# Optimization experiments

Measured on AMD Instinct MI355X. Metric: run time of the kernel, lower is better.

## Reference

```python
import jax, jax.numpy as jnp
import numpy as np

B, T, O = 64, 2048, 3          # batch, window_len, overlap (O >= ngram_n-1)
D, V = 512, 128                # embed_dim, vocab_size
M, NG, H = 100000, 4, 4        # engram memory_size, ngram_n, engram/sgrm num_heads
HD = D // H                    # head_dim = 128
PAD = 0
EPS_RMS = 1e-6


def _engram_primes():
    # per-head rolling-hash primes, exactly as in MultiHeadEngram.setup
    ps = []
    base = 131
    for h in range(H):
        x = base + h * 1009
        row = []
        for _ in range(NG):
            row.append(x)
            x = x * 31 + 1
        ps.append(row)
    return jnp.asarray(np.array(ps, dtype=np.uint32))  # (H, NG)


def setup_inputs() -> dict:
    key = jax.random.key(0)
    ks = jax.random.split(key, 10)
    tokens_w = jax.random.randint(ks[0], (B, T), 0, V, dtype=jnp.int32)
    prev_ids_overlap = jax.random.randint(ks[1], (B, O), 0, V, dtype=jnp.int32)
    mask_bool = jax.random.randint(ks[2], (B, T), 0, 2) > 0
    embed_table = jax.random.normal(ks[3], (V, D), jnp.float32) * 0.02
    engram_table = jax.random.normal(ks[4], (M, H, HD), jnp.float32) * 0.02
    gate_logit = jnp.full((H, HD), -2.0, jnp.float32)
    temp = jnp.ones((H,), jnp.float32)
    sal_W = jax.random.normal(ks[5], (D, H), jnp.float32) * 0.02
    sal_b = jnp.zeros((H,), jnp.float32)
    gate_W = jax.random.normal(ks[6], (HD, 1), jnp.float32) * 0.02
    gate_b = jnp.zeros((1,), jnp.float32)
    rms_scale = jnp.ones((D,), jnp.float32)
    return {"tokens_w": tokens_w, "prev_ids_overlap": prev_ids_overlap,
            "mask_bool": mask_bool, "embed_table": embed_table,
            "engram_table": engram_table, "gate_logit": gate_logit,
            "temp": temp, "sal_W": sal_W, "sal_b": sal_b,
            "gate_W": gate_W, "gate_b": gate_b, "rms_scale": rms_scale}


def reference(tokens_w, prev_ids_overlap, mask_bool, embed_table, engram_table,
              gate_logit, temp, sal_W, sal_b, gate_W, gate_b, rms_scale):
    # ---- MultiHeadEngram: hashed n-gram multi-head gather + sigmoid gate ----
    cur = jnp.where(tokens_w == PAD, 0, tokens_w)
    prv = jnp.where(prev_ids_overlap == PAD, 0, prev_ids_overlap)
    full_seq = jnp.concatenate([prv, cur], axis=1).astype(jnp.uint32)  # (B, O+T)
    primes = _engram_primes()                                          # (H, NG)
    hash_sums = jnp.zeros((B, T, H), dtype=jnp.uint32)
    for i in range(NG):  # rolling n-gram hash (uint32 wraparound)
        chunk = full_seq[:, O - i: O + T - i]                          # (B, T)
        hash_sums = hash_sums + chunk[:, :, None] * primes[None, None, :, i]
    lookup = (hash_sums % M).astype(jnp.int32)                         # (B, T, H)
    # per-head gather: row lookup[b,t,h] of head h's table slice
    retrieved = engram_table[lookup, jnp.arange(H)[None, None, :], :]  # (B, T, H, HD)
    gate = jax.nn.sigmoid(gate_logit)                                  # (H, HD)
    engram_out = (retrieved * gate[None, None]).reshape(B, T, D)

    # token embedding + engram injection (dropout is identity: deterministic)
    x = embed_table[tokens_w] + engram_out                             # (B, T, D)

    # ---- SalienceWriteHead: masked softmax temporal pooling + gating ----
    x_heads = x.reshape(B, T, H, HD)
    temperature = jax.nn.softplus(temp) + 0.3                          # (H,)
    logits = (x @ sal_W + sal_b) / temperature[None, None, :]          # (B, T, H)
    m = mask_bool[:, :, None]
    safe_logits = jnp.where(m, logits, -1e9)
    max_logits = jax.lax.stop_gradient(jnp.max(safe_logits, axis=1, keepdims=True))
    exps = jnp.where(m, jnp.exp(safe_logits - max_logits), 0.0)
    weights = exps / (jnp.sum(exps, axis=1, keepdims=True) + 1e-6)     # (B, T, H)
    write_vec_heads = jnp.einsum('bth,bthd->bhd', weights, x_heads)    # (B, H, HD)
    gate_logits = write_vec_heads @ gate_W + gate_b                    # (B, H, 1)
    window_valid = jnp.any(mask_bool, axis=1)[:, None, None]
    write_u_heads = jax.nn.sigmoid(gate_logits) * window_valid.astype(jnp.float32)
    write_vec = write_vec_heads.reshape(B, D)
    # RMSNorm
    rms = jnp.sqrt(jnp.mean(jnp.square(write_vec), axis=-1, keepdims=True) + EPS_RMS)
    write_vec = write_vec / rms * rms_scale
    write_u_expanded = jnp.tile(write_u_heads, (1, 1, HD)).reshape(B, D)
    return jnp.concatenate([write_vec, write_u_expanded], axis=-1)     # (B, 2D)
```

## Files before the change

kernel.cpp:

```cpp
#include <hip/hip_runtime.h>
#include <stdint.h>

#define B_ 64
#define T_ 2048
#define O_ 3
#define D_ 512
#define V_ 128
#define M_ 100000
#define H_ 4
#define HD_ 128

__device__ __constant__ unsigned PRIMES_c[H_][4] = {
  {131u,  4062u,  125923u, 3903614u},
  {1140u, 35341u, 1095572u, 33962733u},
  {2149u, 66620u, 2065221u, 64021852u},
  {3158u, 97899u, 3034870u, 94080971u},
};

template<int CTRL, int RMASK>
__device__ __forceinline__ float dpp_term(float x) {
  return __int_as_float(__builtin_amdgcn_update_dpp(
      0, __float_as_int(x), CTRL, RMASK, 0xF, true));
}

__device__ __forceinline__ float wave_sum(float x) {
  x += dpp_term<0xB1, 0xF>(x);
  x += dpp_term<0x4E, 0xF>(x);
  x += dpp_term<0x141, 0xF>(x);
  x += dpp_term<0x140, 0xF>(x);
  x += dpp_term<0x142, 0xA>(x);
  x += dpp_term<0x143, 0xC>(x);
  return __int_as_float(__builtin_amdgcn_readlane(__float_as_int(x), 63));
}

__device__ __forceinline__ bool read_mask(const void* mb, size_t i, int imode) {
  return imode ? (((const int*)mb)[i] != 0)
               : (((const unsigned char*)mb)[i] != 0);
}

__device__ __forceinline__ void detect_imode(const void* maskbuf, int tid,
                                             int* s_imode) {
  if (tid < 64) {
    const uint4* mw = (const uint4*)maskbuf;
    unsigned bad = 0;
    #pragma unroll
    for (int i = 0; i < 8; ++i) {
      uint4 v = mw[tid + i * 64];
      bad |= (v.x > 1u) | (v.y > 1u) | (v.z > 1u) | (v.w > 1u);
    }
    unsigned long long anybad = __ballot(bad != 0);
    if (tid == 0) *s_imode = (anybad == 0ull) ? 1 : 0;
  }
}

template<int TC>
__global__ __launch_bounds__(256) void k_pass1(
    const int* __restrict__ tokens, const int* __restrict__ prev,
    const void* __restrict__ maskbuf, const float* __restrict__ embed,
    const float* __restrict__ engram, const float* __restrict__ gate_logit,
    const float* __restrict__ temp, const float* __restrict__ salW,
    const float* __restrict__ salb, float* __restrict__ partials)
{
  const int NCH = T_ / TC;
  int blk = blockIdx.x;
  int b = blk / NCH, c = blk % NCH;
  int t0 = c * TC;
  int tid = threadIdx.x;
  int h = tid >> 6, lane = tid & 63;

  __shared__ int s_imode;
  __shared__ int ltok[TC + 3];
  __shared__ unsigned eoff[TC * H_];
  __shared__ int s_act[TC];
  __shared__ int s_cnt[2];
  __shared__ int s_nact;

  detect_imode(maskbuf, tid, &s_imode);
  for (int j = tid; j < TC + 3; j += 256) {
    int g = t0 + j;
    ltok[j] = (g < O_) ? prev[b * O_ + g] : tokens[(size_t)b * T_ + g - O_];
  }
  __syncthreads();

  int imode = s_imode;
  static_assert(TC == 128, "compaction path assumes TC==128");
  bool act = false;
  unsigned long long bal = 0;
  if (tid < TC) {
    act = read_mask(maskbuf, (size_t)b * T_ + t0 + tid, imode);
    bal = __ballot(act);
    if ((tid & 63) == 0) s_cnt[tid >> 6] = __popcll(bal);
  }
  __syncthreads();
  if (tid < TC) {
    int l = tid & 63;
    int pre = __popcll(bal & ((1ull << l) - 1));
    int base = (tid >> 6) ? s_cnt[0] : 0;
    if (act) s_act[base + pre] = tid;
    if (tid == 0) s_nact = s_cnt[0] + s_cnt[1];
  }
  __syncthreads();
  int nact = s_nact;

  for (int k = tid; k < nact * H_; k += 256) {
    int a  = k >> 2;
    int hh = k & 3;
    int j  = s_act[a];
    unsigned hs = (unsigned)ltok[j + 3] * PRIMES_c[hh][0]
                + (unsigned)ltok[j + 2] * PRIMES_c[hh][1]
                + (unsigned)ltok[j + 1] * PRIMES_c[hh][2]
                + (unsigned)ltok[j]     * PRIMES_c[hh][3];
    unsigned idx = hs % (unsigned)M_;
    eoff[k] = idx * (unsigned)(H_ * HD_) + (unsigned)(hh * HD_);
  }
  __syncthreads();

  int d0 = lane * 2;
  int gd = h * HD_ + d0;
  float g0 = 1.f / (1.f + __expf(-gate_logit[gd]));
  float g1 = 1.f / (1.f + __expf(-gate_logit[gd + 1]));
  float w0 = salW[gd * H_ + h];
  float w1 = salW[(gd + 1) * H_ + h];
  float tv = temp[h];
  float sp = (tv > 20.f) ? tv : log1pf(__expf(tv));
  float invT = 1.f / (sp + 0.3f);
  float sb = salb[h];

  float m = -1e30f, s = 0.f, a0 = 0.f, a1 = 0.f;

  #pragma unroll 4
  for (int k = 0; k < nact; ++k) {
    int j = s_act[k];
    int tokc = ltok[j + 3];
    unsigned eo = eoff[k * H_ + h];
    float2 r = *(const float2*)(engram + eo + d0);
    float2 e = *(const float2*)(embed + tokc * D_ + gd);
    float x0 = fmaf(r.x, g0, e.x);
    float x1 = fmaf(r.y, g1, e.y);
    float pd = x0 * w0 + x1 * w1;
    float dot = wave_sum(pd);
    float logit = (dot + sb) * invT;
    if (logit <= m) {
      float w = __expf(logit - m);
      s += w;
      a0 = fmaf(w, x0, a0);
      a1 = fmaf(w, x1, a1);
    } else {
      float al = __expf(m - logit);
      s  = fmaf(s,  al, 1.f);
      a0 = fmaf(a0, al, x0);
      a1 = fmaf(a1, al, x1);
      m = logit;
    }
  }

  float* P = partials + ((size_t)(b * NCH + c) * H_ + h) * (HD_ + 2);
  if (lane == 0) { P[0] = m; P[1] = s; }
  *(float2*)(P + 2 + d0) = make_float2(a0, a1);
}

template<int TC>
__global__ __launch_bounds__(256) void k_pass2(
    const float* __restrict__ partials, const void* __restrict__ maskbuf,
    const float* __restrict__ gateW, const float* __restrict__ gateb,
    const float* __restrict__ rms_scale, float* __restrict__ out)
{
  const int NCH = T_ / TC;
  int b = blockIdx.x;
  int tid = threadIdx.x, h = tid >> 6, lane = tid & 63;

  __shared__ int s_imode;
  __shared__ int s_any;
  __shared__ float s_ss[H_];
  if (tid == 0) s_any = 0;
  detect_imode(maskbuf, tid, &s_imode);
  __syncthreads();
  int imode = s_imode;
  int any = 0;
  for (int j = tid; j < T_; j += 256)
    any |= read_mask(maskbuf, (size_t)b * T_ + j, imode) ? 1 : 0;
  if (any) s_any = 1;
  __syncthreads();

  int d0 = lane * 2;
  float M = -1e30f;
  for (int c = 0; c < NCH; ++c) {
    const float* P = partials + ((size_t)(b * NCH + c) * H_ + h) * (HD_ + 2);
    M = fmaxf(M, P[0]);
  }
  float S = 0.f, A0 = 0.f, A1 = 0.f;
  for (int c = 0; c < NCH; ++c) {
    const float* P = partials + ((size_t)(b * NCH + c) * H_ + h) * (HD_ + 2);
    float f = __expf(P[0] - M);
    float2 a = *(const float2*)(P + 2 + d0);
    S  = fmaf(P[1], f, S);
    A0 = fmaf(a.x, f, A0);
    A1 = fmaf(a.y, f, A1);
  }
  float inv = 1.f / (S + 1e-6f);
  float v0 = A0 * inv, v1 = A1 * inv;

  float pg = v0 * gateW[d0] + v1 * gateW[d0 + 1];
  float ss = v0 * v0 + v1 * v1;
  float gl  = wave_sum(pg);
  float sst = wave_sum(ss);
  if (lane == 0) s_ss[h] = sst;
  __syncthreads();
  float tot = s_ss[0] + s_ss[1] + s_ss[2] + s_ss[3];
  float rinv = rsqrtf(tot / (float)D_ + 1e-6f);
  float u = (1.f / (1.f + __expf(-(gl + gateb[0])))) * (s_any ? 1.f : 0.f);

  int gd = h * HD_ + d0;
  size_t ob = (size_t)b * (2 * D_);
  out[ob + gd]          = v0 * rinv * rms_scale[gd];
  out[ob + gd + 1]      = v1 * rinv * rms_scale[gd + 1];
  out[ob + D_ + gd]     = u;
  out[ob + D_ + gd + 1] = u;
}

extern "C" void kernel_launch(void* const* d_in, const int* in_sizes, int n_in,
                              void* d_out, int out_size, void* d_ws, size_t ws_size,
                              hipStream_t stream)
{
  const int*   tokens     = (const int*)d_in[0];
  const int*   prev       = (const int*)d_in[1];
  const void*  mask       = d_in[2];
  const float* embed      = (const float*)d_in[3];
  const float* engram     = (const float*)d_in[4];
  const float* gate_logit = (const float*)d_in[5];
  const float* temp       = (const float*)d_in[6];
  const float* salW       = (const float*)d_in[7];
  const float* salb       = (const float*)d_in[8];
  const float* gateW      = (const float*)d_in[9];
  const float* gateb      = (const float*)d_in[10];
  const float* rms_scale  = (const float*)d_in[11];
  float* out = (float*)d_out;

  float* partials = (float*)d_ws;

  k_pass1<128><<<B_ * (T_ / 128), 256, 0, stream>>>(
      tokens, prev, mask, embed, engram, gate_logit, temp, salW, salb,
      partials);
  k_pass2<128><<<B_, 256, 0, stream>>>(
      partials, mask, gateW, gateb, rms_scale, out);
}
```

Before: 318.2 us.

## Fuse passes via last-block atomic reduction and process two tokens per wave

Merges the two kernels into one: each block writes its partial softmax state, bumps a per-batch atomic counter, and the last block for that batch does the final cross-chunk merge, gate and RMSNorm. The main loop now has each half-wave handle a different token with float4 loads and a 32-lane reduction, using a branchless online softmax, and the two halves are merged at the end. The mask-any check is replaced by testing whether the softmax denominator is nonzero. This removes a kernel launch and the second full mask scan, but adds a memset, fences and an atomic, and the tail work is serialized in one block per batch.

```diff
diff --git a/kernel.cpp b/kernel.cpp
--- a/kernel.cpp
+++ b/kernel.cpp
@@ -5,10 +5,12 @@
 #define T_ 2048
 #define O_ 3
 #define D_ 512
-#define V_ 128
 #define M_ 100000
 #define H_ 4
 #define HD_ 128
+#define TC_ 128
+#define NCH_ (T_ / TC_)
+#define PSTR_ 132
 
 __device__ __constant__ unsigned PRIMES_c[H_][4] = {
   {131u,  4062u,  125923u, 3903614u},
@@ -21,6 +23,15 @@
 __device__ __forceinline__ float dpp_term(float x) {
   return __int_as_float(__builtin_amdgcn_update_dpp(
       0, __float_as_int(x), CTRL, RMASK, 0xF, true));
+}
+
+__device__ __forceinline__ float red32(float x) {
+  x += dpp_term<0xB1, 0xF>(x);
+  x += dpp_term<0x4E, 0xF>(x);
+  x += dpp_term<0x141, 0xF>(x);
+  x += dpp_term<0x140, 0xF>(x);
+  x += __shfl_xor(x, 16, 64);
+  return x;
 }
 
 __device__ __forceinline__ float wave_sum(float x) {
@@ -53,51 +64,54 @@
   }
 }
 
-template<int TC>
-__global__ __launch_bounds__(256) void k_pass1(
+__global__ __launch_bounds__(256) void k_fused(
     const int* __restrict__ tokens, const int* __restrict__ prev,
     const void* __restrict__ maskbuf, const float* __restrict__ embed,
     const float* __restrict__ engram, const float* __restrict__ gate_logit,
     const float* __restrict__ temp, const float* __restrict__ salW,
-    const float* __restrict__ salb, float* __restrict__ partials)
+    const float* __restrict__ salb, const float* __restrict__ gateW,
+    const float* __restrict__ gateb, const float* __restrict__ rms_scale,
+    int* __restrict__ cnt, float* __restrict__ partials,
+    float* __restrict__ out)
 {
-  const int NCH = T_ / TC;
   int blk = blockIdx.x;
-  int b = blk / NCH, c = blk % NCH;
-  int t0 = c * TC;
+  int b = blk / NCH_, c = blk % NCH_;
+  int t0 = c * TC_;
   int tid = threadIdx.x;
   int h = tid >> 6, lane = tid & 63;
+  int half = lane >> 5, sl = lane & 31;
 
   __shared__ int s_imode;
-  __shared__ int ltok[TC + 3];
-  __shared__ unsigned eoff[TC * H_];
-  __shared__ int s_act[TC];
-  __shared__ int s_cnt[2];
+  __shared__ int ltok[TC_ + 3];
+  __shared__ unsigned eoff[TC_ * H_];
+  __shared__ int s_act[TC_];
+  __shared__ int s_cnt2[2];
   __shared__ int s_nact;
+  __shared__ int s_last;
+  __shared__ float s_ss[H_];
 
   detect_imode(maskbuf, tid, &s_imode);
-  for (int j = tid; j < TC + 3; j += 256) {
+  for (int j = tid; j < TC_ + 3; j += 256) {
     int g = t0 + j;
     ltok[j] = (g < O_) ? prev[b * O_ + g] : tokens[(size_t)b * T_ + g - O_];
   }
   __syncthreads();
 
   int imode = s_imode;
-  static_assert(TC == 128, "compaction path assumes TC==128");
   bool act = false;
   unsigned long long bal = 0;
-  if (tid < TC) {
+  if (tid < TC_) {
     act = read_mask(maskbuf, (size_t)b * T_ + t0 + tid, imode);
     bal = __ballot(act);
-    if ((tid & 63) == 0) s_cnt[tid >> 6] = __popcll(bal);
-  }
-  __syncthreads();
-  if (tid < TC) {
+    if ((tid & 63) == 0) s_cnt2[tid >> 6] = __popcll(bal);
+  }
+  __syncthreads();
+  if (tid < TC_) {
     int l = tid & 63;
     int pre = __popcll(bal & ((1ull << l) - 1));
-    int base = (tid >> 6) ? s_cnt[0] : 0;
+    int base = (tid >> 6) ? s_cnt2[0] : 0;
     if (act) s_act[base + pre] = tid;
-    if (tid == 0) s_nact = s_cnt[0] + s_cnt[1];
+    if (tid == 0) s_nact = s_cnt2[0] + s_cnt2[1];
   }
   __syncthreads();
   int nact = s_nact;
@@ -115,92 +129,96 @@
   }
   __syncthreads();
 
-  int d0 = lane * 2;
+  int d0 = sl * 4;
   int gd = h * HD_ + d0;
-  float g0 = 1.f / (1.f + __expf(-gate_logit[gd]));
-  float g1 = 1.f / (1.f + __expf(-gate_logit[gd + 1]));
-  float w0 = salW[gd * H_ + h];
+  float4 glv = *(const float4*)(gate_logit + gd);
+  float g0 = 1.f / (1.f + __expf(-glv.x));
+  float g1 = 1.f / (1.f + __expf(-glv.y));
+  float g2 = 1.f / (1.f + __expf(-glv.z));
+  float g3 = 1.f / (1.f + __expf(-glv.w));
+  float w0 = salW[(gd + 0) * H_ + h];
   float w1 = salW[(gd + 1) * H_ + h];
+  float w2 = salW[(gd + 2) * H_ + h];
+  float w3 = salW[(gd + 3) * H_ + h];
   float tv = temp[h];
   float sp = (tv > 20.f) ? tv : log1pf(__expf(tv));
   float invT = 1.f / (sp + 0.3f);
   float sb = salb[h];
 
-  float m = -1e30f, s = 0.f, a0 = 0.f, a1 = 0.f;
-
-  #pragma unroll 4
-  for (int k = 0; k < nact; ++k) {
-    int j = s_act[k];
+  float m = -1e30f, s = 0.f;
+  float a0 = 0.f, a1 = 0.f, a2 = 0.f, a3 = 0.f;
+
+  #pragma unroll 2
+  for (int k = 0; k < nact; k += 2) {
+    int ka = k + half;
+    bool valid = ka < nact;
+    int aidx = valid ? ka : (nact - 1);
+    int j = s_act[aidx];
     int tokc = ltok[j + 3];
-    unsigned eo = eoff[k * H_ + h];
-    float2 r = *(const float2*)(engram + eo + d0);
-    float2 e = *(const float2*)(embed + tokc * D_ + gd);
+    unsigned eo = eoff[aidx * H_ + h];
+    float4 r = *(const float4*)(engram + eo + d0);
+    float4 e = *(const float4*)(embed + tokc * D_ + gd);
     float x0 = fmaf(r.x, g0, e.x);
     float x1 = fmaf(r.y, g1, e.y);
-    float pd = x0 * w0 + x1 * w1;
-    float dot = wave_sum(pd);
-    float logit = (dot + sb) * invT;
-    if (logit <= m) {
-      float w = __expf(logit - m);
-      s += w;
-      a0 = fmaf(w, x0, a0);
-      a1 = fmaf(w, x1, a1);
-    } else {
-      float al = __expf(m - logit);
-      s  = fmaf(s,  al, 1.f);
-      a0 = fmaf(a0, al, x0);
-      a1 = fmaf(a1, al, x1);
-      m = logit;
-    }
-  }
-
-  float* P = partials + ((size_t)(b * NCH + c) * H_ + h) * (HD_ + 2);
-  if (lane == 0) { P[0] = m; P[1] = s; }
-  *(float2*)(P + 2 + d0) = make_float2(a0, a1);
-}
-
-template<int TC>
-__global__ __launch_bounds__(256) void k_pass2(
-    const float* __restrict__ partials, const void* __restrict__ maskbuf,
-    const float* __restrict__ gateW, const float* __restrict__ gateb,
-    const float* __restrict__ rms_scale, float* __restrict__ out)
-{
-  const int NCH = T_ / TC;
-  int b = blockIdx.x;
-  int tid = threadIdx.x, h = tid >> 6, lane = tid & 63;
-
-  __shared__ int s_imode;
-  __shared__ int s_any;
-  __shared__ float s_ss[H_];
-  if (tid == 0) s_any = 0;
-  detect_imode(maskbuf, tid, &s_imode);
-  __syncthreads();
-  int imode = s_imode;
-  int any = 0;
-  for (int j = tid; j < T_; j += 256)
-    any |= read_mask(maskbuf, (size_t)b * T_ + j, imode) ? 1 : 0;
-  if (any) s_any = 1;
-  __syncthreads();
-
-  int d0 = lane * 2;
+    float x2 = fmaf(r.z, g2, e.z);
+    float x3 = fmaf(r.w, g3, e.w);
+    float pd = fmaf(x3, w3, fmaf(x2, w2, fmaf(x1, w1, x0 * w0)));
+    float dot = red32(pd);
+    float logit = valid ? (dot + sb) * invT : -1e30f;
+    float nm = fmaxf(m, logit);
+    float al = __expf(m - nm);
+    float w  = __expf(logit - nm);
+    s  = fmaf(s,  al, w);
+    a0 = fmaf(a0, al, w * x0);
+    a1 = fmaf(a1, al, w * x1);
+    a2 = fmaf(a2, al, w * x2);
+    a3 = fmaf(a3, al, w * x3);
+    m = nm;
+  }
+  float pm = __shfl_xor(m, 32, 64);
+  float M2 = fmaxf(m, pm);
+  float fs = __expf(m - M2);
+  float fp = __expf(pm - M2);
+  float S2 = fmaf(s, fs, __shfl_xor(s, 32, 64) * fp);
+  float A0 = fmaf(a0, fs, __shfl_xor(a0, 32, 64) * fp);
+  float A1 = fmaf(a1, fs, __shfl_xor(a1, 32, 64) * fp);
+  float A2 = fmaf(a2, fs, __shfl_xor(a2, 32, 64) * fp);
+  float A3 = fmaf(a3, fs, __shfl_xor(a3, 32, 64) * fp);
+
+  float* P = partials + ((size_t)(b * NCH_ + c) * H_ + h) * PSTR_;
+  if (half == 0) {
+    *(float4*)(P + d0) = make_float4(A0, A1, A2, A3);
+    if (sl == 0) { P[HD_] = M2; P[HD_ + 1] = S2; }
+  }
+
+  __threadfence();
+  __syncthreads();
+  if (tid == 0) {
+    int old = atomicAdd(&cnt[b], 1);
+    s_last = (old == NCH_ - 1) ? 1 : 0;
+  }
+  __syncthreads();
+  if (!s_last) return;
+  __threadfence();
+
+  int d0f = lane * 2;
+  const float* Pb = partials + (size_t)b * NCH_ * H_ * PSTR_;
   float M = -1e30f;
-  for (int c = 0; c < NCH; ++c) {
-    const float* P = partials + ((size_t)(b * NCH + c) * H_ + h) * (HD_ + 2);
-    M = fmaxf(M, P[0]);
-  }
-  float S = 0.f, A0 = 0.f, A1 = 0.f;
-  for (int c = 0; c < NCH; ++c) {
-    const float* P = partials + ((size_t)(b * NCH + c) * H_ + h) * (HD_ + 2);
-    float f = __expf(P[0] - M);
-    float2 a = *(const float2*)(P + 2 + d0);
-    S  = fmaf(P[1], f, S);
-    A0 = fmaf(a.x, f, A0);
-    A1 = fmaf(a.y, f, A1);
+  for (int cc = 0; cc < NCH_; ++cc)
+    M = fmaxf(M, Pb[(cc * H_ + h) * PSTR_ + HD_]);
+  float S = 0.f, B0 = 0.f, B1 = 0.f;
+  for (int cc = 0; cc < NCH_; ++cc) {
+    const float* Pc = Pb + (cc * H_ + h) * PSTR_;
+    float f = __expf(Pc[HD_] - M);
+    float2 a = *(const float2*)(Pc + d0f);
+    S  = fmaf(Pc[HD_ + 1], f, S);
+    B0 = fmaf(a.x, f, B0);
+    B1 = fmaf(a.y, f, B1);
   }
   float inv = 1.f / (S + 1e-6f);
-  float v0 = A0 * inv, v1 = A1 * inv;
-
-  float pg = v0 * gateW[d0] + v1 * gateW[d0 + 1];
+  float v0 = B0 * inv, v1 = B1 * inv;
+
+  float pg = v0 * gateW[d0f] + v1 * gateW[d0f + 1];
   float ss = v0 * v0 + v1 * v1;
   float gl  = wave_sum(pg);
   float sst = wave_sum(ss);
@@ -208,14 +226,15 @@
   __syncthreads();
   float tot = s_ss[0] + s_ss[1] + s_ss[2] + s_ss[3];
   float rinv = rsqrtf(tot / (float)D_ + 1e-6f);
-  float u = (1.f / (1.f + __expf(-(gl + gateb[0])))) * (s_any ? 1.f : 0.f);
-
-  int gd = h * HD_ + d0;
+  float anyf = (S > 0.5f) ? 1.f : 0.f;
+  float u = (1.f / (1.f + __expf(-(gl + gateb[0])))) * anyf;
+
+  int gdf = h * HD_ + d0f;
   size_t ob = (size_t)b * (2 * D_);
-  out[ob + gd]          = v0 * rinv * rms_scale[gd];
-  out[ob + gd + 1]      = v1 * rinv * rms_scale[gd + 1];
-  out[ob + D_ + gd]     = u;
-  out[ob + D_ + gd + 1] = u;
+  out[ob + gdf]          = v0 * rinv * rms_scale[gdf];
+  out[ob + gdf + 1]      = v1 * rinv * rms_scale[gdf + 1];
+  out[ob + D_ + gdf]     = u;
+  out[ob + D_ + gdf + 1] = u;
 }
 
 extern "C" void kernel_launch(void* const* d_in, const int* in_sizes, int n_in,
@@ -236,11 +255,11 @@
   const float* rms_scale  = (const float*)d_in[11];
   float* out = (float*)d_out;
 
-  float* partials = (float*)d_ws;
-
-  k_pass1<128><<<B_ * (T_ / 128), 256, 0, stream>>>(
+  int*   cnt      = (int*)d_ws;
+  float* partials = (float*)((char*)d_ws + 256);
+
+  hipMemsetAsync(cnt, 0, 256, stream);
+  k_fused<<<B_ * NCH_, 256, 0, stream>>>(
       tokens, prev, mask, embed, engram, gate_logit, temp, salW, salb,
-      partials);
-  k_pass2<128><<<B_, 256, 0, stream>>>(
-      partials, mask, gateW, gateb, rms_scale, out);
-}
+      gateW, gateb, rms_scale, cnt, partials, out);
+}
```

New measurement: 431.7 us. +35.7%, slower.
